# Performance work log

Hardware: AMD Instinct MI355X
Metric: run time of the kernel (lower is better)

Reference implementation:

```python
import jax, jax.numpy as jnp
import numpy as np

N, D, E, NNZ = 200000, 128, 1024, 1600000


def setup_inputs() -> dict:
    key = jax.random.key(0)
    ks = jax.random.split(key, 8)
    x = jax.random.normal(ks[0], (N, D), jnp.float32)
    tb_W = jax.random.normal(ks[1], (5, 3, D, D), jnp.float32) * 0.05
    tb_b = jax.random.normal(ks[2], (5, 3, D), jnp.float32) * 0.05
    hg_W = jax.random.normal(ks[3], (2, D, D), jnp.float32) * 0.05
    hg_b = jax.random.normal(ks[4], (2, D), jnp.float32) * 0.05
    hyperedge_attr = jax.random.normal(ks[5], (E, D), jnp.float32)
    node_idx = jax.random.randint(ks[6], (NNZ,), 0, N)
    edge_idx = jax.random.randint(ks[7], (NNZ,), 0, E)
    return dict(x=x, tb_W=tb_W, tb_b=tb_b, hg_W=hg_W, hg_b=hg_b,
                hyperedge_attr=hyperedge_attr, node_idx=node_idx,
                edge_idx=edge_idx, num_hyperedges=E)


def _time_block(x, W, b):
    # 1x1 Conv2d over channel dim == per-node linear. W:[3,D,D], b:[3,D]
    c1 = x @ W[0] + b[0]
    c2 = x @ W[1] + b[1]
    c3 = x @ W[2] + b[2]
    return jax.nn.relu(c1 + jax.nn.sigmoid(c2) + c3)


def _hypergraph_conv(x, node_idx, edge_idx, W, b, num_nodes, num_edges):
    # PyG HypergraphConv, use_attention=False (heads=1):
    # out = D^{-1} H B H^T (x W) + b, H given as COO (node_idx, edge_idx)
    xp = x @ W
    ones = jnp.ones(node_idx.shape[0], xp.dtype)
    Dn = jax.ops.segment_sum(ones, node_idx, num_segments=num_nodes)
    Dn = jnp.where(Dn > 0, 1.0 / Dn, 0.0)
    Be = jax.ops.segment_sum(ones, edge_idx, num_segments=num_edges)
    Be = jnp.where(Be > 0, 1.0 / Be, 0.0)
    # node -> hyperedge aggregation, normalized by 1/B_e
    m = jax.ops.segment_sum(xp[node_idx], edge_idx, num_segments=num_edges) * Be[:, None]
    # hyperedge -> node aggregation, normalized by 1/D_v
    out = jax.ops.segment_sum(m[edge_idx], node_idx, num_segments=num_nodes) * Dn[:, None]
    return out + b


def reference(x, tb_W, tb_b, hg_W, hg_b, hyperedge_attr, node_idx, edge_idx, num_hyperedges):
    # hyperedge_attr is unused when use_attention=False (faithful to PyG)
    n = x.shape[0]
    h = _time_block(x, tb_W[0], tb_b[0])
    h = _hypergraph_conv(h, node_idx, edge_idx, hg_W[0], hg_b[0], n, num_hyperedges)
    h = _time_block(h, tb_W[1], tb_b[1])
    h = _time_block(h, tb_W[2], tb_b[2])
    h = _hypergraph_conv(h, node_idx, edge_idx, hg_W[1], hg_b[1], n, num_hyperedges)
    h = _time_block(h, tb_W[3], tb_b[3])
    h = _time_block(h, tb_W[4], tb_b[4])
    return h
```

## Files before the change

### kernel.cpp

```cpp
#include <hip/hip_runtime.h>
#include <stdint.h>

#define N_NODES 200000
#define DIM     128
#define N_EDGES 1024
#define NNZ_C   1600000
#define NT_TILES 6250

#define NBLK   250
#define CHUNK  6400
#define ITERS  25
#define NCB    196

#define NG_BLOCKS 2000
#define NG_WAVES  (NG_BLOCKS*4)
#define NG_K      25
#define NG_STAGE  512

typedef __attribute__((ext_vector_type(8))) short short8;
typedef __attribute__((ext_vector_type(4))) float f32x4;

__device__ __forceinline__ float u2f(uint32_t u){ union{uint32_t u;float f;} x; x.u=u; return x.f; }
__device__ __forceinline__ uint32_t f2u(float f){ union{uint32_t u;float f;} x; x.f=f; return x.u; }
__device__ __forceinline__ unsigned short f2bf(float f){
  uint32_t u = f2u(f);
  u += 0x7fffu + ((u >> 16) & 1u);
  return (unsigned short)(u >> 16);
}

__global__ void prep_tb_w(const float* __restrict__ W, short* __restrict__ Wt){
  int i = blockIdx.x*256 + threadIdx.x;
  if (i >= 5*384*128) return;
  int k   = i & 127;
  int col = (i >> 7) % 384;
  int s   = i / 49152;
  int j = col >> 7, n = col & 127;
  Wt[i] = (short)f2bf(W[((s*3 + j)*128 + k)*128 + n]);
}
__global__ void prep_hg_wf(const float* __restrict__ W, float* __restrict__ Wtf){
  int i = blockIdx.x*256 + threadIdx.x;
  if (i >= 2*128*128) return;
  int k = i & 127;
  int n = (i >> 7) & 127;
  int g = i >> 14;
  Wtf[i] = W[(g*128 + k)*128 + n];
}

__global__ __launch_bounds__(256) void hist_kernel(
    const int* __restrict__ nidx, const int* __restrict__ eidx,
    int* __restrict__ ebh, int* __restrict__ nbh)
{
  __shared__ int eh[N_EDGES];
  __shared__ int nh[NCB];
  int tid = threadIdx.x, blk = blockIdx.x;
  #pragma unroll
  for (int l = tid; l < N_EDGES; l += 256) eh[l] = 0;
  for (int l = tid; l < NCB; l += 256) nh[l] = 0;
  __syncthreads();
  int base = blk*CHUNK;
  for (int it = 0; it < ITERS; it++){
    int i = base + it*256 + tid;
    atomicAdd(&eh[eidx[i]], 1);
    atomicAdd(&nh[nidx[i] >> 10], 1);
  }
  __syncthreads();
  for (int l = tid; l < N_EDGES; l += 256) ebh[blk*N_EDGES + l] = eh[l];
  for (int l = tid; l < NCB; l += 256) nbh[blk*NCB + l] = nh[l];
}

__global__ __launch_bounds__(1024) void escan_kernel(
    int* __restrict__ ebh, int* __restrict__ eoff)
{
  __shared__ int sc[1024];
  int e = threadIdx.x;
  int total = 0;
  #pragma unroll 10
  for (int b = 0; b < NBLK; b++){
    int idx = b*N_EDGES + e;
    int t = ebh[idx];
    ebh[idx] = total;
    total += t;
  }
  sc[e] = total; __syncthreads();
  for (int off=1; off<1024; off<<=1){
    int v = (e >= off) ? sc[e-off] : 0;
    __syncthreads();
    sc[e] += v;
    __syncthreads();
  }
  int base = sc[e] - total;
  eoff[e] = base;
  if (e == 1023) eoff[1024] = sc[1023];
  #pragma unroll 10
  for (int b = 0; b < NBLK; b++) ebh[b*N_EDGES + e] += base;
}

__global__ __launch_bounds__(256) void nscan_kernel(
    int* __restrict__ nbh, int* __restrict__ cbase)
{
  __shared__ int sc[256];
  int c = threadIdx.x;
  int total = 0;
  if (c < NCB){
    #pragma unroll 10
    for (int b = 0; b < NBLK; b++){
      int idx = b*NCB + c;
      int t = nbh[idx];
      nbh[idx] = total;
      total += t;
    }
  }
  sc[c] = (c < NCB) ? total : 0; __syncthreads();
  for (int off=1; off<256; off<<=1){
    int v = (c >= off) ? sc[c-off] : 0;
    __syncthreads();
    sc[c] += v;
    __syncthreads();
  }
  int base = sc[c] - ((c < NCB) ? total : 0);
  if (c < NCB) cbase[c] = base;
  if (c == NCB-1) cbase[NCB] = sc[c];
  __syncthreads();
  if (c < NCB){
    #pragma unroll 10
    for (int b = 0; b < NBLK; b++) nbh[b*NCB + c] += base;
  }
}

__global__ __launch_bounds__(256) void scatter_kernel(
    const int* __restrict__ nidx, const int* __restrict__ eidx,
    const int* __restrict__ ebh, const int* __restrict__ nbh,
    int* __restrict__ enodes, uint32_t* __restrict__ pairs)
{
  __shared__ int cure[N_EDGES];
  __shared__ int curn[NCB];
  int tid = threadIdx.x, blk = blockIdx.x;
  for (int l = tid; l < N_EDGES; l += 256) cure[l] = ebh[blk*N_EDGES + l];
  for (int l = tid; l < NCB; l += 256)     curn[l] = nbh[blk*NCB + l];
  __syncthreads();
  int base = blk*CHUNK;
  for (int it = 0; it < ITERS; it++){
    int i = base + it*256 + tid;
    int v = nidx[i], e = eidx[i];
    int pe = atomicAdd(&cure[e], 1);
    enodes[pe] = v;
    int pn = atomicAdd(&curn[v >> 10], 1);
    pairs[pn] = ((uint32_t)v << 10) | (uint32_t)e;
  }
}

__global__ __launch_bounds__(256) void node_build_kernel(
    const uint32_t* __restrict__ pairs, const int* __restrict__ cbase,
    int* __restrict__ noff, int* __restrict__ nedges)
{
  __shared__ int cnt[1024];
  __shared__ int off[1024];
  __shared__ int part[256];
  int tid = threadIdx.x, c = blockIdx.x;
  int n0 = c << 10;
  int nloc = min(1024, N_NODES - n0);
  int s = cbase[c], e = cbase[c+1];
  #pragma unroll
  for (int l = tid; l < 1024; l += 256) cnt[l] = 0;
  __syncthreads();
  for (int i = s + tid; i < e; i += 256)
    atomicAdd(&cnt[(pairs[i] >> 10) & 1023], 1);
  __syncthreads();
  int c0 = cnt[tid*4], c1 = cnt[tid*4+1], c2 = cnt[tid*4+2], c3 = cnt[tid*4+3];
  int sum = c0+c1+c2+c3;
  part[tid] = sum; __syncthreads();
  for (int o=1; o<256; o<<=1){
    int v = (tid >= o) ? part[tid-o] : 0;
    __syncthreads();
    part[tid] += v;
    __syncthreads();
  }
  int pb = part[tid] - sum;
  off[tid*4]   = pb;
  off[tid*4+1] = pb + c0;
  off[tid*4+2] = pb + c0 + c1;
  off[tid*4+3] = pb + c0 + c1 + c2;
  __syncthreads();
  for (int l = tid; l < nloc; l += 256) noff[n0 + l] = s + off[l];
  if (c == 0 && tid == 0) noff[N_NODES] = NNZ_C;
  __syncthreads();
  for (int i = s + tid; i < e; i += 256){
    uint32_t p = pairs[i];
    int local = (p >> 10) & 1023;
    int pos = s + atomicAdd(&off[local], 1);
    nedges[pos] = (int)((p & 1023) << 8);
  }
}

template<bool IN_F32, int OUT_MODE>
__global__ __launch_bounds__(256, 2) void gemm_kernel(
    const void* __restrict__ in, void* __restrict__ out,
    const short* __restrict__ Wt, const float* __restrict__ bias)
{
  __shared__ short Atile[32][136];
  const int tid  = threadIdx.x;
  const int lane = tid & 63;
  const int w    = tid >> 6;
  const int l15  = lane & 15;
  const int quad = lane >> 4;

  short8 bfrag[3][2][4];
  #pragma unroll
  for (int j = 0; j < 3; j++)
    #pragma unroll
    for (int nt = 0; nt < 2; nt++){
      const short* bp = Wt + (j*128 + w*32 + nt*16 + l15)*128 + quad*8;
      #pragma unroll
      for (int ks = 0; ks < 4; ks++)
        bfrag[j][nt][ks] = *(const short8*)(bp + ks*32);
    }

  float bv[3][2];
  #pragma unroll
  for (int j = 0; j < 3; j++)
    #pragma unroll
    for (int nt = 0; nt < 2; nt++)
      bv[j][nt] = bias[j*128 + w*32 + nt*16 + l15];

  const int arow = tid >> 3;
  const int aseg = (tid & 7) * 2;

  short8 pre0, pre1;
  auto loadA = [&](int t){
    int off = (t*32 + arow)*128 + aseg*8;
    if (IN_F32){
      const float* f = (const float*)in + off;
      f32x4 q0 = ((const f32x4*)f)[0];
      f32x4 q1 = ((const f32x4*)f)[1];
      f32x4 q2 = ((const f32x4*)f)[2];
      f32x4 q3 = ((const f32x4*)f)[3];
      short8 t0, t1;
      #pragma unroll
      for (int u = 0; u < 4; u++){
        t0[u]   = (short)f2bf(q0[u]);
        t0[u+4] = (short)f2bf(q1[u]);
        t1[u]   = (short)f2bf(q2[u]);
        t1[u+4] = (short)f2bf(q3[u]);
      }
      pre0 = t0; pre1 = t1;
    } else {
      const short* hp = (const short*)in + off;
      pre0 = *(const short8*)hp;
      pre1 = *(const short8*)(hp + 8);
    }
  };

  int t = blockIdx.x;
  loadA(t);
  for (;;){
    __syncthreads();
    *(short8*)&Atile[arow][aseg*8]     = pre0;
    *(short8*)&Atile[arow][aseg*8 + 8] = pre1;
    __syncthreads();
    int tn = t + gridDim.x;
    if (tn < NT_TILES) loadA(tn);

    const int base = t*32;
    #pragma unroll
    for (int rt = 0; rt < 2; rt++){
      short8 af[4];
      #pragma unroll
      for (int ks = 0; ks < 4; ks++)
        af[ks] = *(const short8*)&Atile[rt*16 + l15][ks*32 + quad*8];

      f32x4 acc[3][2];
      #pragma unroll
      for (int j = 0; j < 3; j++)
        #pragma unroll
        for (int nt = 0; nt < 2; nt++){
          acc[j][nt] = (f32x4){0.f, 0.f, 0.f, 0.f};
          #pragma unroll
          for (int ks = 0; ks < 4; ks++)
            acc[j][nt] = __builtin_amdgcn_mfma_f32_16x16x32_bf16(
                af[ks], bfrag[j][nt][ks], acc[j][nt], 0, 0, 0);
        }

      #pragma unroll
      for (int nt = 0; nt < 2; nt++){
        int col = w*32 + nt*16 + l15;
        #pragma unroll
        for (int r = 0; r < 4; r++){
          int row = base + rt*16 + quad*4 + r;
          float c2 = acc[1][nt][r] + bv[1][nt];
          float sg = 1.f / (1.f + __expf(-c2));
          float v = acc[0][nt][r] + bv[0][nt] + sg + acc[2][nt][r] + bv[2][nt];
          v = fmaxf(v, 0.f);
          if (OUT_MODE == 1) ((float*)out)[row*128 + col] = v;
          else if (OUT_MODE == 0) ((unsigned short*)out)[row*128 + col] = f2bf(v);
          else {
            int pk = __builtin_amdgcn_cvt_pk_fp8_f32(v, v, 0, false);
            ((unsigned char*)out)[row*128 + col] = (unsigned char)(pk & 0xff);
          }
        }
      }
    }
    if (tn >= NT_TILES) break;
    t = tn;
  }
}

__device__ __forceinline__ void acc16(float* a, uint4 r){
  uint32_t w[4] = {r.x, r.y, r.z, r.w};
  #pragma unroll
  for (int q = 0; q < 4; q++){
    auto lo = __builtin_amdgcn_cvt_pk_f32_fp8(w[q], false);
    auto hi = __builtin_amdgcn_cvt_pk_f32_fp8(w[q], true);
    a[q*4+0] += lo[0]; a[q*4+1] += lo[1]; a[q*4+2] += hi[0]; a[q*4+3] += hi[1];
  }
}

__global__ __launch_bounds__(256) void edge_gather_kernel(
    const unsigned char* __restrict__ h8, const int* __restrict__ eoff,
    const int* __restrict__ enodes, float* __restrict__ s_e)
{
  int e = blockIdx.x;
  int s = eoff[e], en = eoff[e+1];
  int tid  = threadIdx.x;
  int slot = tid >> 3;
  int ch   = tid & 7;
  const size_t choff = (size_t)ch * 16;

  float a[16];
  #pragma unroll
  for (int j = 0; j < 16; j++) a[j] = 0.f;

  int i0 = s + slot;
  int n0 = (i0      < en) ? enodes[i0]      : -1;
  int n1 = (i0 + 32 < en) ? enodes[i0 + 32] : -1;
  int n2 = (i0 + 64 < en) ? enodes[i0 + 64] : -1;
  int n3 = (i0 + 96 < en) ? enodes[i0 + 96] : -1;

  while (i0 < en){
    int i1 = i0 + 128;
    int m0 = (i1      < en) ? enodes[i1]      : -1;
    int m1 = (i1 + 32 < en) ? enodes[i1 + 32] : -1;
    int m2 = (i1 + 64 < en) ? enodes[i1 + 64] : -1;
    int m3 = (i1 + 96 < en) ? enodes[i1 + 96] : -1;

    uint4 r0 = *(const uint4*)(h8 + (((size_t)max(n0,0)) << 7) + choff);
    uint4 r1 = *(const uint4*)(h8 + (((size_t)max(n1,0)) << 7) + choff);
    uint4 r2 = *(const uint4*)(h8 + (((size_t)max(n2,0)) << 7) + choff);
    uint4 r3 = *(const uint4*)(h8 + (((size_t)max(n3,0)) << 7) + choff);
    if (n0 < 0) r0 = make_uint4(0,0,0,0);
    if (n1 < 0) r1 = make_uint4(0,0,0,0);
    if (n2 < 0) r2 = make_uint4(0,0,0,0);
    if (n3 < 0) r3 = make_uint4(0,0,0,0);

    acc16(a, r0); acc16(a, r1); acc16(a, r2); acc16(a, r3);

    n0 = m0; n1 = m1; n2 = m2; n3 = m3;
    i0 = i1;
  }

  __shared__ float red[32][132];
  #pragma unroll
  for (int j = 0; j < 16; j++) red[slot][ch*16 + j] = a[j];
  __syncthreads();
  if (tid < 128){
    float sum = 0.f;
    #pragma unroll
    for (int r = 0; r < 32; r++) sum += red[r][tid];
    s_e[e*128 + tid] = sum;
  }
}

__global__ __launch_bounds__(128) void egemm_kernel(
    const float* __restrict__ s_e, const int* __restrict__ eoff,
    const float* __restrict__ Wtf, uint32_t* __restrict__ mbf)
{
  __shared__ float srow[128];
  __shared__ float sacc[128];
  int e = blockIdx.x, n = threadIdx.x;
  srow[n] = s_e[e*128 + n];
  __syncthreads();
  int deg = eoff[e+1] - eoff[e];
  float be = deg > 0 ? 1.f/(float)deg : 0.f;
  const f32x4* w4 = (const f32x4*)(Wtf + n*128);
  float acc = 0.f;
  #pragma unroll
  for (int k = 0; k < 32; k++){
    f32x4 qv = w4[k];
    acc += qv[0]*srow[k*4] + qv[1]*srow[k*4+1] + qv[2]*srow[k*4+2] + qv[3]*srow[k*4+3];
  }
  sacc[n] = acc * be;
  __syncthreads();
  if (n < 64){
    uint32_t lo = f2bf(sacc[2*n]);
    uint32_t hi = f2bf(sacc[2*n+1]);
    mbf[e*64 + n] = (hi << 16) | lo;
  }
}

__global__ __launch_bounds__(256) void node_gather_kernel(
    const uint32_t* __restrict__ mbf, const int* __restrict__ noff,
    const int* __restrict__ nedges, const float* __restrict__ hb,
    uint32_t* __restrict__ outp)
{
  __shared__ int sidx[4][NG_STAGE];
  const int wslot = threadIdx.x >> 6;
  const int wid   = (blockIdx.x << 2) | wslot;
  const int lane  = threadIdx.x & 63;
  const int lane4 = lane << 2;
  const float b0 = hb[2*lane], b1 = hb[2*lane+1];
  const int v0 = wid * NG_K;

  int eArr = noff[min(v0 + 1 + lane, N_NODES)];
  int sW   = __builtin_amdgcn_readfirstlane(noff[v0]);
  int send = __builtin_amdgcn_readlane(eArr, NG_K - 1);
  int n = send - sW;

  int* myIdx = sidx[wslot];
  bool useLds = (n <= NG_STAGE);
  if (useLds){
    for (int b = lane; b < n; b += 64) myIdx[b] = nedges[sW + b];
  }
  __syncthreads();

  const char* mb = (const char*)mbf;
  if (useLds){
    int s = sW;
    for (int vr = 0; vr < NG_K; vr++){
      int e = __builtin_amdgcn_readlane(eArr, vr);
      float a0 = 0.f, a1 = 0.f;
      uint32_t rlast = 0;
      for (int i = s; i < e; i += 8){
        uint32_t r[8];
        #pragma unroll
        for (int k = 0; k < 8; k++){
          int li = min(i + k, e - 1) - sW;
          r[k] = *(const uint32_t*)(mb + (myIdx[li] + lane4));
        }
        #pragma unroll
        for (int k = 0; k < 8; k++){
          a0 += u2f(r[k] << 16);
          a1 += u2f(r[k] & 0xffff0000u);
        }
        rlast = r[7];
      }
      int d = e - s;
      float dead = (float)(((d + 7) & ~7) - d);
      a0 -= dead * u2f(rlast << 16);
      a1 -= dead * u2f(rlast & 0xffff0000u);
      float dn = (d > 0) ? 1.f/(float)d : 0.f;
      uint32_t lo = f2bf(a0*dn + b0);
      uint32_t hi = f2bf(a1*dn + b1);
      outp[((size_t)(v0 + vr) << 6) | lane] = (hi << 16) | lo;
      s = e;
    }
  } else {
    int s = sW;
    for (int vr = 0; vr < NG_K; vr++){
      int e = __builtin_amdgcn_readlane(eArr, vr);
      float a0 = 0.f, a1 = 0.f;
      for (int i = s; i < e; i++){
        uint32_t r = *(const uint32_t*)(mb + (nedges[i] + lane4));
        a0 += u2f(r << 16);
        a1 += u2f(r & 0xffff0000u);
      }
      int d = e - s;
      float dn = (d > 0) ? 1.f/(float)d : 0.f;
      uint32_t lo = f2bf(a0*dn + b0);
      uint32_t hi = f2bf(a1*dn + b1);
      outp[((size_t)(v0 + vr) << 6) | lane] = (hi << 16) | lo;
      s = e;
    }
  }
}

extern "C" void kernel_launch(void* const* d_in, const int* in_sizes, int n_in,
                              void* d_out, int out_size, void* d_ws, size_t ws_size,
                              hipStream_t stream)
{
  (void)in_sizes; (void)n_in; (void)out_size; (void)ws_size;
  const float* x   = (const float*)d_in[0];
  const float* tbW = (const float*)d_in[1];
  const float* tbb = (const float*)d_in[2];
  const float* hgW = (const float*)d_in[3];
  const float* hgb = (const float*)d_in[4];
  const int* nidx  = (const int*)d_in[6];
  const int* eidx  = (const int*)d_in[7];
  float* out = (float*)d_out;

  char* p = (char*)d_ws;
  auto alloc = [&](size_t sz){ void* r = (void*)p; p += (sz + 255) & ~(size_t)255; return r; };
  unsigned short* hA = (unsigned short*)alloc((size_t)N_NODES*DIM*2);
  unsigned short* hB = (unsigned short*)alloc((size_t)N_NODES*DIM*2);
  unsigned char*  h8 = (unsigned char*)alloc((size_t)N_NODES*DIM);
  float* s_e  = (float*)alloc((size_t)N_EDGES*DIM*4);
  uint32_t* mbf = (uint32_t*)alloc((size_t)N_EDGES*64*4);
  short* WtTb = (short*)alloc((size_t)5*384*128*2);
  float* Wtf  = (float*)alloc((size_t)2*128*128*4);
  int* ebh  = (int*)alloc((size_t)NBLK*N_EDGES*4);
  int* nbh  = (int*)alloc((size_t)NBLK*NCB*4);
  int* eoff = (int*)alloc((N_EDGES+1)*4);
  int* cbase= (int*)alloc((NCB+1)*4);
  int* noff = (int*)alloc((size_t)(N_NODES+1)*4);
  int* enodes = (int*)alloc((size_t)NNZ_C*4);
  int* nedges = (int*)alloc((size_t)NNZ_C*4 + 64);
  uint32_t* pairs = (uint32_t*)h8;

  prep_tb_w<<<960, 256, 0, stream>>>(tbW, WtTb);
  prep_hg_wf<<<128, 256, 0, stream>>>(hgW, Wtf);

  hist_kernel<<<NBLK, 256, 0, stream>>>(nidx, eidx, ebh, nbh);
  escan_kernel<<<1, 1024, 0, stream>>>(ebh, eoff);
  nscan_kernel<<<1, 256, 0, stream>>>(nbh, cbase);
  scatter_kernel<<<NBLK, 256, 0, stream>>>(nidx, eidx, ebh, nbh, enodes, pairs);
  node_build_kernel<<<NCB, 256, 0, stream>>>(pairs, cbase, noff, nedges);

  gemm_kernel<true, 2><<<1024, 256, 0, stream>>>(x, h8, WtTb, tbb);
  edge_gather_kernel<<<N_EDGES, 256, 0, stream>>>(h8, eoff, enodes, s_e);
  egemm_kernel<<<N_EDGES, 128, 0, stream>>>(s_e, eoff, Wtf, mbf);
  node_gather_kernel<<<NG_BLOCKS, 256, 0, stream>>>(mbf, noff, nedges, hgb, (uint32_t*)hA);
  gemm_kernel<false, 0><<<1024, 256, 0, stream>>>(hA, hB, WtTb + 1*49152, tbb + 1*384);
  gemm_kernel<false, 2><<<1024, 256, 0, stream>>>(hB, h8, WtTb + 2*49152, tbb + 2*384);
  edge_gather_kernel<<<N_EDGES, 256, 0, stream>>>(h8, eoff, enodes, s_e);
  egemm_kernel<<<N_EDGES, 128, 0, stream>>>(s_e, eoff, Wtf + 16384, mbf);
  node_gather_kernel<<<NG_BLOCKS, 256, 0, stream>>>(mbf, noff, nedges, hgb + 128, (uint32_t*)hA);
  gemm_kernel<false, 0><<<1024, 256, 0, stream>>>(hA, hB, WtTb + 3*49152, tbb + 3*384);
  gemm_kernel<false, 1><<<1024, 256, 0, stream>>>(hB, out, WtTb + 4*49152, tbb + 4*384);
}
```

Baseline: 655.5 us.

## Fuse consecutive time-block GEMM pairs into one kernel keeping intermediate in LDS

```diff
diff --git a/kernel.cpp b/kernel.cpp
--- a/kernel.cpp
+++ b/kernel.cpp
@@ -16,6 +16,9 @@
 #define NG_WAVES  (NG_BLOCKS*4)
 #define NG_K      25
 #define NG_STAGE  512
+
+#define G2_TPB   5
+#define G2_GRID  1250
 
 typedef __attribute__((ext_vector_type(8))) short short8;
 typedef __attribute__((ext_vector_type(4))) float f32x4;
@@ -301,6 +304,136 @@
     }
     if (tn >= NT_TILES) break;
     t = tn;
+  }
+}
+
+template<int OUT_MODE>
+__global__ __launch_bounds__(256, 2) void gemm2_kernel(
+    const unsigned short* __restrict__ in, void* __restrict__ out,
+    const short* __restrict__ WtA, const float* __restrict__ biasA,
+    const short* __restrict__ WtB, const float* __restrict__ biasB)
+{
+  __shared__ short Atile[32][136];
+  __shared__ short h1[G2_TPB][32][136];
+  const int tid  = threadIdx.x;
+  const int lane = tid & 63;
+  const int w    = tid >> 6;
+  const int l15  = lane & 15;
+  const int quad = lane >> 4;
+
+  short8 bfrag[3][2][4];
+  float bv[3][2];
+  auto loadW = [&](const short* Wt, const float* bias){
+    #pragma unroll
+    for (int j = 0; j < 3; j++)
+      #pragma unroll
+      for (int nt = 0; nt < 2; nt++){
+        const short* bp = Wt + (j*128 + w*32 + nt*16 + l15)*128 + quad*8;
+        #pragma unroll
+        for (int ks = 0; ks < 4; ks++)
+          bfrag[j][nt][ks] = *(const short8*)(bp + ks*32);
+        bv[j][nt] = bias[j*128 + w*32 + nt*16 + l15];
+      }
+  };
+  loadW(WtA, biasA);
+
+  const int arow = tid >> 3;
+  const int aseg = (tid & 7) * 2;
+  const int t0 = blockIdx.x * G2_TPB;
+
+  short8 pre0, pre1;
+  auto loadA = [&](int g){
+    const short* hp = (const short*)in + ((t0 + g)*32 + arow)*128 + aseg*8;
+    pre0 = *(const short8*)hp;
+    pre1 = *(const short8*)(hp + 8);
+  };
+
+  loadA(0);
+  #pragma unroll 1
+  for (int g = 0; g < G2_TPB; g++){
+    __syncthreads();
+    *(short8*)&Atile[arow][aseg*8]     = pre0;
+    *(short8*)&Atile[arow][aseg*8 + 8] = pre1;
+    __syncthreads();
+    if (g + 1 < G2_TPB) loadA(g + 1);
+
+    #pragma unroll
+    for (int rt = 0; rt < 2; rt++){
+      short8 af[4];
+      #pragma unroll
+      for (int ks = 0; ks < 4; ks++)
+        af[ks] = *(const short8*)&Atile[rt*16 + l15][ks*32 + quad*8];
+
+      f32x4 acc[3][2];
+      #pragma unroll
+      for (int j = 0; j < 3; j++)
+        #pragma unroll
+        for (int nt = 0; nt < 2; nt++){
+          acc[j][nt] = (f32x4){0.f, 0.f, 0.f, 0.f};
+          #pragma unroll
+          for (int ks = 0; ks < 4; ks++)
+            acc[j][nt] = __builtin_amdgcn_mfma_f32_16x16x32_bf16(
+                af[ks], bfrag[j][nt][ks], acc[j][nt], 0, 0, 0);
+        }
+
+      #pragma unroll
+      for (int nt = 0; nt < 2; nt++){
+        int col = w*32 + nt*16 + l15;
+        #pragma unroll
+        for (int r = 0; r < 4; r++){
+          int row = rt*16 + quad*4 + r;
+          float c2 = acc[1][nt][r] + bv[1][nt];
+          float sg = 1.f / (1.f + __expf(-c2));
+          float v = acc[0][nt][r] + bv[0][nt] + sg + acc[2][nt][r] + bv[2][nt];
+          h1[g][row][col] = (short)f2bf(fmaxf(v, 0.f));
+        }
+      }
+    }
+  }
+
+  loadW(WtB, biasB);
+  __syncthreads();
+
+  #pragma unroll 1
+  for (int g = 0; g < G2_TPB; g++){
+    const int base = (t0 + g)*32;
+    #pragma unroll
+    for (int rt = 0; rt < 2; rt++){
+      short8 af[4];
+      #pragma unroll
+      for (int ks = 0; ks < 4; ks++)
+        af[ks] = *(const short8*)&h1[g][rt*16 + l15][ks*32 + quad*8];
+
+      f32x4 acc[3][2];
+      #pragma unroll
+      for (int j = 0; j < 3; j++)
+        #pragma unroll
+        for (int nt = 0; nt < 2; nt++){
+          acc[j][nt] = (f32x4){0.f, 0.f, 0.f, 0.f};
+          #pragma unroll
+          for (int ks = 0; ks < 4; ks++)
+            acc[j][nt] = __builtin_amdgcn_mfma_f32_16x16x32_bf16(
+                af[ks], bfrag[j][nt][ks], acc[j][nt], 0, 0, 0);
+        }
+
+      #pragma unroll
+      for (int nt = 0; nt < 2; nt++){
+        int col = w*32 + nt*16 + l15;
+        #pragma unroll
+        for (int r = 0; r < 4; r++){
+          int row = base + rt*16 + quad*4 + r;
+          float c2 = acc[1][nt][r] + bv[1][nt];
+          float sg = 1.f / (1.f + __expf(-c2));
+          float v = acc[0][nt][r] + bv[0][nt] + sg + acc[2][nt][r] + bv[2][nt];
+          v = fmaxf(v, 0.f);
+          if (OUT_MODE == 1) ((float*)out)[row*128 + col] = v;
+          else {
+            int pk = __builtin_amdgcn_cvt_pk_fp8_f32(v, v, 0, false);
+            ((unsigned char*)out)[row*128 + col] = (unsigned char)(pk & 0xff);
+          }
+        }
+      }
+    }
   }
 }
 
@@ -489,7 +622,6 @@
   char* p = (char*)d_ws;
   auto alloc = [&](size_t sz){ void* r = (void*)p; p += (sz + 255) & ~(size_t)255; return r; };
   unsigned short* hA = (unsigned short*)alloc((size_t)N_NODES*DIM*2);
-  unsigned short* hB = (unsigned short*)alloc((size_t)N_NODES*DIM*2);
   unsigned char*  h8 = (unsigned char*)alloc((size_t)N_NODES*DIM);
   float* s_e  = (float*)alloc((size_t)N_EDGES*DIM*4);
   uint32_t* mbf = (uint32_t*)alloc((size_t)N_EDGES*64*4);
@@ -517,11 +649,11 @@
   edge_gather_kernel<<<N_EDGES, 256, 0, stream>>>(h8, eoff, enodes, s_e);
   egemm_kernel<<<N_EDGES, 128, 0, stream>>>(s_e, eoff, Wtf, mbf);
   node_gather_kernel<<<NG_BLOCKS, 256, 0, stream>>>(mbf, noff, nedges, hgb, (uint32_t*)hA);
-  gemm_kernel<false, 0><<<1024, 256, 0, stream>>>(hA, hB, WtTb + 1*49152, tbb + 1*384);
-  gemm_kernel<false, 2><<<1024, 256, 0, stream>>>(hB, h8, WtTb + 2*49152, tbb + 2*384);
+  gemm2_kernel<2><<<G2_GRID, 256, 0, stream>>>(hA, h8,
+      WtTb + 1*49152, tbb + 1*384, WtTb + 2*49152, tbb + 2*384);
   edge_gather_kernel<<<N_EDGES, 256, 0, stream>>>(h8, eoff, enodes, s_e);
   egemm_kernel<<<N_EDGES, 128, 0, stream>>>(s_e, eoff, Wtf + 16384, mbf);
   node_gather_kernel<<<NG_BLOCKS, 256, 0, stream>>>(mbf, noff, nedges, hgb + 128, (uint32_t*)hA);
-  gemm_kernel<false, 0><<<1024, 256, 0, stream>>>(hA, hB, WtTb + 3*49152, tbb + 3*384);
-  gemm_kernel<false, 1><<<1024, 256, 0, stream>>>(hB, out, WtTb + 4*49152, tbb + 4*384);
-}
+  gemm2_kernel<1><<<G2_GRID, 256, 0, stream>>>(hA, out,
+      WtTb + 3*49152, tbb + 3*384, WtTb + 4*49152, tbb + 4*384);
+}
```

New measurement: 673.7 us. 1.03x slower.
